# Performance work log

Measured on AMD Instinct MI355X. Metric: run time of the kernel, lower is better.

## Reference

```python
import jax, jax.numpy as jnp
import numpy as np

N_NODES = 100000
N_COMM = 1024
N_EDGES = 3200000
D_IN = 128
D_OUT = 128


def setup_inputs() -> dict:
    key = jax.random.key(0)
    k1, k2, k3, k4, k5, k6 = jax.random.split(key, 6)
    x = jax.random.normal(k1, (N_NODES + N_COMM, D_IN), dtype=jnp.float32)
    weight = jax.random.normal(k2, (D_IN, D_OUT), dtype=jnp.float32) * (1.0 / np.sqrt(D_IN))
    # assignments must be positive so row/col sums are nonzero
    assignments = jax.random.uniform(k3, (N_NODES, N_COMM), dtype=jnp.float32)
    edge_row = jax.random.randint(k4, (N_EDGES,), 0, N_NODES, dtype=jnp.int32)
    edge_col = jax.random.randint(k5, (N_EDGES,), 0, N_NODES, dtype=jnp.int32)
    edge_val = jax.random.uniform(k6, (N_EDGES,), dtype=jnp.float32)
    return {"x": x, "weight": weight, "assignments": assignments,
            "edge_row": edge_row, "edge_col": edge_col, "edge_val": edge_val}


def reference(x, weight, assignments, edge_row, edge_col, edge_val):
    N, C = assignments.shape
    support = x @ weight                      # [N+C, D_OUT]
    sup_nodes = support[:N]                   # node rows (support[:-C])
    sup_comm = support[N:]                    # community rows (support[-C:])

    # row-normalized assignments @ community support
    a_norm = assignments / assignments.sum(axis=1, keepdims=True)  # [N, C]
    comm_to_node = a_norm @ sup_comm                               # [N, D_OUT]

    # sparse adj @ node support via COO gather + segment scatter-add
    msgs = edge_val[:, None] * sup_nodes[edge_col]                 # [E, D_OUT]
    spmm = jax.ops.segment_sum(msgs, edge_row, num_segments=N)     # [N, D_OUT]

    output1 = comm_to_node + spmm                                  # [N, D_OUT]

    # row-normalized assignments.T @ node support
    at = assignments.T                                             # [C, N]
    at_norm = at / at.sum(axis=1, keepdims=True)
    output2 = at_norm @ sup_nodes                                  # [C, D_OUT]

    return jnp.concatenate((output1, output2), axis=0)            # [N+C, D_OUT]
```

## Files before the change

kernel.cpp:

```cpp
#include <hip/hip_runtime.h>

#define NN 100000
#define NC 1024
#define NM 101024
#define NE 3200000
#define DD 128

typedef __attribute__((ext_vector_type(8))) short s16x8;
typedef __attribute__((ext_vector_type(4))) float f32x4;

#define MFMA __builtin_amdgcn_mfma_f32_16x16x32_bf16

__device__ __forceinline__ short f2bf(float f) {
  unsigned u = __float_as_uint(f);
  u = (u + 0x7FFFu + ((u >> 16) & 1u)) >> 16;
  return (short)u;
}
__device__ __forceinline__ float bf2f(short h) {
  return __uint_as_float(((unsigned)(unsigned short)h) << 16);
}

__global__ __launch_bounds__(256) void k_zero(int* __restrict__ p, int n) {
  int t = blockIdx.x * 256 + threadIdx.x;
  if (t < n) p[t] = 0;
}

__global__ __launch_bounds__(256) void k_wpack(const float* __restrict__ W,
                                               short* __restrict__ wh,
                                               short* __restrict__ wl) {
  int t = blockIdx.x * 256 + threadIdx.x;
  int k = t >> 7, d = t & 127;
  float v = W[t];
  short h = f2bf(v);
  short l = f2bf(v - bf2f(h));
  int idx = (((k >> 5) * 8 + (d >> 4)) * 64 + ((k >> 3) & 3) * 16 + (d & 15)) * 8 + (k & 7);
  wh[idx] = h;
  wl[idx] = l;
}

__global__ __launch_bounds__(256) void k_support(const float* __restrict__ x,
                                                 const short* __restrict__ wh,
                                                 const short* __restrict__ wl,
                                                 float* __restrict__ sup) {
  int wave = threadIdx.x >> 6, lane = threadIdx.x & 63;
  int r0 = blockIdx.x * 64 + wave * 16;
  int arow = r0 + (lane & 15);
  if (arow >= NM) arow = NM - 1;
  int kb = (lane >> 4) * 8;
  f32x4 acc[8];
  #pragma unroll
  for (int dt = 0; dt < 8; ++dt)
    #pragma unroll
    for (int q = 0; q < 4; ++q) acc[dt][q] = 0.f;

  #pragma unroll
  for (int ks = 0; ks < 4; ++ks) {
    const float* ap = x + (size_t)arow * DD + ks * 32 + kb;
    float4 v0 = *(const float4*)ap;
    float4 v1 = *(const float4*)(ap + 4);
    float vv[8] = {v0.x, v0.y, v0.z, v0.w, v1.x, v1.y, v1.z, v1.w};
    s16x8 xh, xl;
    #pragma unroll
    for (int j = 0; j < 8; ++j) {
      short h = f2bf(vv[j]);
      xh[j] = h;
      xl[j] = f2bf(vv[j] - bf2f(h));
    }
    const short* bph = wh + ks * 4096 + lane * 8;
    const short* bpl = wl + ks * 4096 + lane * 8;
    #pragma unroll
    for (int dt = 0; dt < 8; ++dt) {
      s16x8 bh = *(const s16x8*)(bph + dt * 512);
      s16x8 bl = *(const s16x8*)(bpl + dt * 512);
      acc[dt] = MFMA(xh, bh, acc[dt], 0, 0, 0);
      acc[dt] = MFMA(xl, bh, acc[dt], 0, 0, 0);
      acc[dt] = MFMA(xh, bl, acc[dt], 0, 0, 0);
    }
  }
  int rg = (lane >> 4) * 4, cc = lane & 15;
  #pragma unroll
  for (int dt = 0; dt < 8; ++dt)
    #pragma unroll
    for (int q = 0; q < 4; ++q) {
      int rr = r0 + rg + q;
      if (rr < NM) sup[(size_t)rr * DD + dt * 16 + cc] = acc[dt][q];
    }
}

__global__ __launch_bounds__(256) void k_spack(const float* __restrict__ sup,
                                               short* __restrict__ bpk) {
  int t = blockIdx.x * 256 + threadIdx.x;
  int d = t & 127, ib = t >> 7;
  int rb = ib >> 2, g = ib & 3;
  s16x8 o;
  #pragma unroll
  for (int j = 0; j < 8; ++j) o[j] = f2bf(sup[(size_t)(ib * 8 + j) * DD + d]);
  *(s16x8*)(bpk + (size_t)((rb * 8 + (d >> 4)) * 64 + g * 16 + (d & 15)) * 8) = o;
}

__global__ __launch_bounds__(256) void k_u1(const float* __restrict__ A,
                                            const short* __restrict__ bpk,
                                            float* __restrict__ out) {
  __shared__ float rsh[128];
  int wave = threadIdx.x >> 6, lane = threadIdx.x & 63;
  int r0 = blockIdx.x * 128 + wave * 32;
  int kb = (lane >> 4) * 8;
  f32x4 acc[2][8];
  #pragma unroll
  for (int m = 0; m < 2; ++m)
    #pragma unroll
    for (int dt = 0; dt < 8; ++dt)
      #pragma unroll
      for (int q = 0; q < 4; ++q) acc[m][dt][q] = 0.f;
  float rs[2] = {0.f, 0.f};
  int row[2];
  #pragma unroll
  for (int m = 0; m < 2; ++m) {
    int r = r0 + m * 16 + (lane & 15);
    row[m] = (r < NN) ? r : NN - 1;
  }
  for (int ks = 0; ks < 32; ++ks) {
    s16x8 af[2];
    #pragma unroll
    for (int m = 0; m < 2; ++m) {
      const float* ap = A + (size_t)row[m] * NC + ks * 32 + kb;
      float4 v0 = *(const float4*)ap;
      float4 v1 = *(const float4*)(ap + 4);
      rs[m] += v0.x + v0.y + v0.z + v0.w + v1.x + v1.y + v1.z + v1.w;
      af[m][0] = f2bf(v0.x); af[m][1] = f2bf(v0.y);
      af[m][2] = f2bf(v0.z); af[m][3] = f2bf(v0.w);
      af[m][4] = f2bf(v1.x); af[m][5] = f2bf(v1.y);
      af[m][6] = f2bf(v1.z); af[m][7] = f2bf(v1.w);
    }
    const short* bp = bpk + (size_t)(3125 + ks) * 4096 + lane * 8;
    #pragma unroll
    for (int dt = 0; dt < 8; ++dt) {
      s16x8 b = *(const s16x8*)(bp + dt * 512);
      acc[0][dt] = MFMA(af[0], b, acc[0][dt], 0, 0, 0);
      acc[1][dt] = MFMA(af[1], b, acc[1][dt], 0, 0, 0);
    }
  }
  #pragma unroll
  for (int m = 0; m < 2; ++m) {
    float v = rs[m];
    v += __shfl_xor(v, 16);
    v += __shfl_xor(v, 32);
    if (lane < 16) rsh[wave * 32 + m * 16 + lane] = v;
  }
  __syncthreads();
  int rg = (lane >> 4) * 4, cc = lane & 15;
  #pragma unroll
  for (int m = 0; m < 2; ++m)
    #pragma unroll
    for (int q = 0; q < 4; ++q) {
      int wr = wave * 32 + m * 16 + rg + q;
      int r = blockIdx.x * 128 + wr;
      if (r < NN) {
        float inv = 1.f / rsh[wr];
        #pragma unroll
        for (int dt = 0; dt < 8; ++dt)
          out[(size_t)r * DD + dt * 16 + cc] = acc[m][dt][q] * inv;
      }
    }
}

__global__ __launch_bounds__(256) void k_u2(const float* __restrict__ A,
                                            const short* __restrict__ bpk,
                                            float* __restrict__ u2,
                                            float* __restrict__ csum) {
  __shared__ short atile[128 * 40];
  int wave = threadIdx.x >> 6, lane = threadIdx.x & 63;
  int c0 = (blockIdx.x & 7) * 128;
  int s = blockIdx.x >> 3;
  int wc = wave * 32;
  f32x4 acc[2][8];
  #pragma unroll
  for (int m = 0; m < 2; ++m)
    #pragma unroll
    for (int dt = 0; dt < 8; ++dt)
      #pragma unroll
      for (int q = 0; q < 4; ++q) acc[m][dt][q] = 0.f;
  float cs[2] = {0.f, 0.f};
  int ld_i = threadIdx.x >> 5;
  int ld_c = (threadIdx.x & 31) * 4;

  for (int kk = 0; kk < 25; ++kk) {
    int i0 = s * 800 + kk * 32;
    __syncthreads();
    #pragma unroll
    for (int it = 0; it < 4; ++it) {
      int i = it * 8 + ld_i;
      float4 v = *(const float4*)(A + (size_t)(i0 + i) * NC + c0 + ld_c);
      atile[(ld_c + 0) * 40 + i] = f2bf(v.x);
      atile[(ld_c + 1) * 40 + i] = f2bf(v.y);
      atile[(ld_c + 2) * 40 + i] = f2bf(v.z);
      atile[(ld_c + 3) * 40 + i] = f2bf(v.w);
    }
    __syncthreads();
    s16x8 af[2];
    #pragma unroll
    for (int m = 0; m < 2; ++m) {
      af[m] = *(const s16x8*)(atile + (wc + m * 16 + (lane & 15)) * 40 + (lane >> 4) * 8);
      #pragma unroll
      for (int j = 0; j < 8; ++j) cs[m] += bf2f(af[m][j]);
    }
    const short* bp = bpk + (size_t)(s * 25 + kk) * 4096 + lane * 8;
    #pragma unroll
    for (int dt = 0; dt < 8; ++dt) {
      s16x8 b = *(const s16x8*)(bp + dt * 512);
      acc[0][dt] = MFMA(af[0], b, acc[0][dt], 0, 0, 0);
      acc[1][dt] = MFMA(af[1], b, acc[1][dt], 0, 0, 0);
    }
  }
  #pragma unroll
  for (int m = 0; m < 2; ++m) {
    float v = cs[m];
    v += __shfl_xor(v, 16);
    v += __shfl_xor(v, 32);
    if (lane < 16) atomicAdd(&csum[c0 + wc + m * 16 + lane], v);
  }
  int rg = (lane >> 4) * 4, cc = lane & 15;
  #pragma unroll
  for (int m = 0; m < 2; ++m)
    #pragma unroll
    for (int dt = 0; dt < 8; ++dt)
      #pragma unroll
      for (int q = 0; q < 4; ++q)
        atomicAdd(&u2[(size_t)(c0 + wc + m * 16 + rg + q) * DD + dt * 16 + cc],
                  acc[m][dt][q]);
}

__global__ __launch_bounds__(256) void k_out2(const float* __restrict__ u2,
                                              const float* __restrict__ csum,
                                              float* __restrict__ out) {
  int t = blockIdx.x * 256 + threadIdx.x;
  int c = t >> 7;
  out[(size_t)(NN + c) * DD + (t & 127)] = u2[t] / csum[c];
}

__global__ __launch_bounds__(256) void k_hist(const int* __restrict__ er, int* __restrict__ hist) {
  int t = blockIdx.x * 256 + threadIdx.x;
  if (t < NE) atomicAdd(&hist[er[t]], 1);
}

__global__ __launch_bounds__(256) void k_scan1(const int* __restrict__ hist,
                                               int* __restrict__ excl,
                                               int* __restrict__ bsum) {
  __shared__ int sm[256];
  int t = threadIdx.x, g = blockIdx.x * 256 + t;
  int v = (g < NN) ? hist[g] : 0;
  sm[t] = v;
  __syncthreads();
  for (int off = 1; off < 256; off <<= 1) {
    int u = (t >= off) ? sm[t - off] : 0;
    __syncthreads();
    sm[t] += u;
    __syncthreads();
  }
  if (g < NN) excl[g] = sm[t] - v;
  if (t == 255) bsum[blockIdx.x] = sm[255];
}

__global__ __launch_bounds__(512) void k_scan2(const int* __restrict__ bsum,
                                               int* __restrict__ boff, int nb) {
  __shared__ int sm[512];
  int t = threadIdx.x;
  int v = (t < nb) ? bsum[t] : 0;
  sm[t] = v;
  __syncthreads();
  for (int off = 1; off < 512; off <<= 1) {
    int u = (t >= off) ? sm[t - off] : 0;
    __syncthreads();
    sm[t] += u;
    __syncthreads();
  }
  if (t < nb) boff[t] = sm[t] - v;
}

__global__ __launch_bounds__(256) void k_scan3(const int* __restrict__ excl,
                                               const int* __restrict__ boff,
                                               int* __restrict__ offs,
                                               int* __restrict__ cur) {
  int t = threadIdx.x, g = blockIdx.x * 256 + t;
  if (g < NN) {
    int o = excl[g] + boff[blockIdx.x];
    offs[g] = o;
    cur[g] = o;
  }
  if (g == 0) offs[NN] = NE;
}

__global__ __launch_bounds__(256) void k_scatter(const int* __restrict__ er,
                                                 const int* __restrict__ ec,
                                                 const float* __restrict__ ev,
                                                 int* __restrict__ cur,
                                                 int2* __restrict__ pairs) {
  int t = blockIdx.x * 256 + threadIdx.x;
  if (t < NE) {
    int r = er[t];
    int p = atomicAdd(&cur[r], 1);
    pairs[p] = make_int2(ec[t], __float_as_int(ev[t]));
  }
}

__global__ __launch_bounds__(256) void k_spmm(const int* __restrict__ offs,
                                              const int2* __restrict__ pairs,
                                              const float* __restrict__ sup,
                                              float* __restrict__ out) {
  int wave = threadIdx.x >> 6, lane = threadIdx.x & 63;
  int row = blockIdx.x * 4 + wave;
  int beg = offs[row], end = offs[row + 1];
  float ax = 0.f, ay = 0.f;
  for (int e = beg; e < end; ++e) {
    int2 p = pairs[e];
    float2 v = *(const float2*)(sup + (size_t)p.x * DD + lane * 2);
    float val = __int_as_float(p.y);
    ax = fmaf(val, v.x, ax);
    ay = fmaf(val, v.y, ay);
  }
  float2* o = (float2*)(out + (size_t)row * DD);
  float2 c = o[lane];
  c.x += ax;
  c.y += ay;
  o[lane] = c;
}

extern "C" void kernel_launch(void* const* d_in, const int* in_sizes, int n_in,
                              void* d_out, int out_size, void* d_ws, size_t ws_size,
                              hipStream_t stream) {
  const float* x  = (const float*)d_in[0];
  const float* W  = (const float*)d_in[1];
  const float* A  = (const float*)d_in[2];
  const int*   er = (const int*)d_in[3];
  const int*   ec = (const int*)d_in[4];
  const float* ev = (const float*)d_in[5];
  float* out = (float*)d_out;

  char* ws = (char*)d_ws;
  size_t off = 0;
  auto alloc = [&](size_t bytes) -> void* {
    off = (off + 255) & ~(size_t)255;
    void* p = ws + off;
    off += bytes;
    return p;
  };
  float* sup   = (float*)alloc((size_t)NM * DD * 4);
  short* bpk   = (short*)alloc((size_t)NM * DD * 2);
  short* wh    = (short*)alloc(128 * 128 * 2);
  short* wl    = (short*)alloc(128 * 128 * 2);
  float* u2    = (float*)alloc((size_t)NC * DD * 4);
  float* csum  = (float*)alloc(NC * 4);
  int*   hist  = (int*)alloc(NN * 4);
  int*   excl  = (int*)alloc(NN * 4);
  int*   offs  = (int*)alloc((NN + 1) * 4);
  int*   cur   = (int*)alloc(NN * 4);
  int*   bsum  = (int*)alloc(512 * 4);
  int*   boff  = (int*)alloc(512 * 4);
  int2*  pairs = (int2*)alloc((size_t)NE * 8);
  (void)ws_size; (void)in_sizes; (void)n_in; (void)out_size;

  const int ZN = NC * DD + NC + NN;
  k_zero<<<dim3((ZN + 255) / 256), dim3(256), 0, stream>>>((int*)u2, ZN);
  k_wpack<<<dim3(64), dim3(256), 0, stream>>>(W, wh, wl);
  k_support<<<dim3(1579), dim3(256), 0, stream>>>(x, wh, wl, sup);
  k_spack<<<dim3(6314), dim3(256), 0, stream>>>(sup, bpk);
  k_hist<<<dim3(12500), dim3(256), 0, stream>>>(er, hist);
  k_scan1<<<dim3(391), dim3(256), 0, stream>>>(hist, excl, bsum);
  k_scan2<<<dim3(1), dim3(512), 0, stream>>>(bsum, boff, 391);
  k_scan3<<<dim3(391), dim3(256), 0, stream>>>(excl, boff, offs, cur);
  k_scatter<<<dim3(12500), dim3(256), 0, stream>>>(er, ec, ev, cur, pairs);
  k_u1<<<dim3(782), dim3(256), 0, stream>>>(A, bpk, out);
  k_u2<<<dim3(1000), dim3(256), 0, stream>>>(A, bpk, u2, csum);
  k_out2<<<dim3(512), dim3(256), 0, stream>>>(u2, csum, out);
  k_spmm<<<dim3(25000), dim3(256), 0, stream>>>(offs, pairs, sup, out);
}
```

Before: 1.647 ms.

## Gather fp16 node support in SpMM, unroll edges, double-buffer k_u2 tiles

Adds a kernel that converts node support rows to packed fp16, and switches the SpMM gather to read these half-size rows, cutting random-gather bandwidth. The SpMM edge loop is unrolled by four so several gathers are in flight at once. k_u2 now double-buffers its LDS tile, prefetching the next A tile into registers while the current one is used, which removes one barrier per iteration. The costs are an extra conversion pass over the support matrix and fp16 rounding of the SpMM inputs, which adds precision loss.

```diff
diff --git a/kernel.cpp b/kernel.cpp
--- a/kernel.cpp
+++ b/kernel.cpp
@@ -1,4 +1,5 @@
 #include <hip/hip_runtime.h>
+#include <hip/hip_fp16.h>
 
 #define NN 100000
 #define NC 1024
@@ -87,6 +88,14 @@
     }
 }
 
+__global__ __launch_bounds__(256) void k_suph(const float* __restrict__ sup,
+                                              unsigned* __restrict__ suph) {
+  int t = blockIdx.x * 256 + threadIdx.x;
+  float2 f = *(const float2*)(sup + (size_t)t * 2);
+  __half2 h = __floats2half2_rn(f.x, f.y);
+  suph[t] = *(unsigned*)&h;
+}
+
 __global__ __launch_bounds__(256) void k_spack(const float* __restrict__ sup,
                                                short* __restrict__ bpk) {
   int t = blockIdx.x * 256 + threadIdx.x;
@@ -168,7 +177,7 @@
                                             const short* __restrict__ bpk,
                                             float* __restrict__ u2,
                                             float* __restrict__ csum) {
-  __shared__ short atile[128 * 40];
+  __shared__ short atile[2][128 * 40];
   int wave = threadIdx.x >> 6, lane = threadIdx.x & 63;
   int c0 = (blockIdx.x & 7) * 128;
   int s = blockIdx.x >> 3;
@@ -184,25 +193,44 @@
   int ld_i = threadIdx.x >> 5;
   int ld_c = (threadIdx.x & 31) * 4;
 
+  float4 rv[4];
+  #pragma unroll
+  for (int it = 0; it < 4; ++it)
+    rv[it] = *(const float4*)(A + (size_t)(s * 800 + it * 8 + ld_i) * NC + c0 + ld_c);
+  #pragma unroll
+  for (int it = 0; it < 4; ++it) {
+    int i = it * 8 + ld_i;
+    atile[0][(ld_c + 0) * 40 + i] = f2bf(rv[it].x);
+    atile[0][(ld_c + 1) * 40 + i] = f2bf(rv[it].y);
+    atile[0][(ld_c + 2) * 40 + i] = f2bf(rv[it].z);
+    atile[0][(ld_c + 3) * 40 + i] = f2bf(rv[it].w);
+  }
+  __syncthreads();
+
   for (int kk = 0; kk < 25; ++kk) {
-    int i0 = s * 800 + kk * 32;
-    __syncthreads();
-    #pragma unroll
-    for (int it = 0; it < 4; ++it) {
-      int i = it * 8 + ld_i;
-      float4 v = *(const float4*)(A + (size_t)(i0 + i) * NC + c0 + ld_c);
-      atile[(ld_c + 0) * 40 + i] = f2bf(v.x);
-      atile[(ld_c + 1) * 40 + i] = f2bf(v.y);
-      atile[(ld_c + 2) * 40 + i] = f2bf(v.z);
-      atile[(ld_c + 3) * 40 + i] = f2bf(v.w);
-    }
-    __syncthreads();
+    int p = kk & 1;
+    if (kk < 24) {
+      int i0n = s * 800 + (kk + 1) * 32;
+      #pragma unroll
+      for (int it = 0; it < 4; ++it)
+        rv[it] = *(const float4*)(A + (size_t)(i0n + it * 8 + ld_i) * NC + c0 + ld_c);
+    }
     s16x8 af[2];
     #pragma unroll
     for (int m = 0; m < 2; ++m) {
-      af[m] = *(const s16x8*)(atile + (wc + m * 16 + (lane & 15)) * 40 + (lane >> 4) * 8);
+      af[m] = *(const s16x8*)(&atile[p][(wc + m * 16 + (lane & 15)) * 40 + (lane >> 4) * 8]);
       #pragma unroll
       for (int j = 0; j < 8; ++j) cs[m] += bf2f(af[m][j]);
+    }
+    if (kk < 24) {
+      #pragma unroll
+      for (int it = 0; it < 4; ++it) {
+        int i = it * 8 + ld_i;
+        atile[p ^ 1][(ld_c + 0) * 40 + i] = f2bf(rv[it].x);
+        atile[p ^ 1][(ld_c + 1) * 40 + i] = f2bf(rv[it].y);
+        atile[p ^ 1][(ld_c + 2) * 40 + i] = f2bf(rv[it].z);
+        atile[p ^ 1][(ld_c + 3) * 40 + i] = f2bf(rv[it].w);
+      }
     }
     const short* bp = bpk + (size_t)(s * 25 + kk) * 4096 + lane * 8;
     #pragma unroll
@@ -211,6 +239,7 @@
       acc[0][dt] = MFMA(af[0], b, acc[0][dt], 0, 0, 0);
       acc[1][dt] = MFMA(af[1], b, acc[1][dt], 0, 0, 0);
     }
+    __syncthreads();
   }
   #pragma unroll
   for (int m = 0; m < 2; ++m) {
@@ -305,18 +334,37 @@
 
 __global__ __launch_bounds__(256) void k_spmm(const int* __restrict__ offs,
                                               const int2* __restrict__ pairs,
-                                              const float* __restrict__ sup,
+                                              const unsigned* __restrict__ suph,
                                               float* __restrict__ out) {
   int wave = threadIdx.x >> 6, lane = threadIdx.x & 63;
   int row = blockIdx.x * 4 + wave;
   int beg = offs[row], end = offs[row + 1];
   float ax = 0.f, ay = 0.f;
-  for (int e = beg; e < end; ++e) {
+  int e = beg;
+  for (; e + 4 <= end; e += 4) {
+    int2 p0 = pairs[e], p1 = pairs[e + 1], p2 = pairs[e + 2], p3 = pairs[e + 3];
+    unsigned g0 = suph[(size_t)p0.x * 64 + lane];
+    unsigned g1 = suph[(size_t)p1.x * 64 + lane];
+    unsigned g2 = suph[(size_t)p2.x * 64 + lane];
+    unsigned g3 = suph[(size_t)p3.x * 64 + lane];
+    float2 v0 = __half22float2(*(__half2*)&g0);
+    float2 v1 = __half22float2(*(__half2*)&g1);
+    float2 v2 = __half22float2(*(__half2*)&g2);
+    float2 v3 = __half22float2(*(__half2*)&g3);
+    float c0 = __int_as_float(p0.y), c1 = __int_as_float(p1.y);
+    float c2 = __int_as_float(p2.y), c3 = __int_as_float(p3.y);
+    ax = fmaf(c0, v0.x, ax); ay = fmaf(c0, v0.y, ay);
+    ax = fmaf(c1, v1.x, ax); ay = fmaf(c1, v1.y, ay);
+    ax = fmaf(c2, v2.x, ax); ay = fmaf(c2, v2.y, ay);
+    ax = fmaf(c3, v3.x, ax); ay = fmaf(c3, v3.y, ay);
+  }
+  for (; e < end; ++e) {
     int2 p = pairs[e];
-    float2 v = *(const float2*)(sup + (size_t)p.x * DD + lane * 2);
-    float val = __int_as_float(p.y);
-    ax = fmaf(val, v.x, ax);
-    ay = fmaf(val, v.y, ay);
+    unsigned g = suph[(size_t)p.x * 64 + lane];
+    float2 v = __half22float2(*(__half2*)&g);
+    float c = __int_as_float(p.y);
+    ax = fmaf(c, v.x, ax);
+    ay = fmaf(c, v.y, ay);
   }
   float2* o = (float2*)(out + (size_t)row * DD);
   float2 c = o[lane];
@@ -344,10 +392,11 @@
     off += bytes;
     return p;
   };
-  float* sup   = (float*)alloc((size_t)NM * DD * 4);
-  short* bpk   = (short*)alloc((size_t)NM * DD * 2);
-  short* wh    = (short*)alloc(128 * 128 * 2);
-  short* wl    = (short*)alloc(128 * 128 * 2);
+  float*    sup   = (float*)alloc((size_t)NM * DD * 4);
+  short*    bpk   = (short*)alloc((size_t)NM * DD * 2);
+  unsigned* suphp = (unsigned*)alloc((size_t)NN * 64 * 4);
+  short*    wh    = (short*)alloc(128 * 128 * 2);
+  short*    wl    = (short*)alloc(128 * 128 * 2);
   float* u2    = (float*)alloc((size_t)NC * DD * 4);
   float* csum  = (float*)alloc(NC * 4);
   int*   hist  = (int*)alloc(NN * 4);
@@ -363,6 +412,7 @@
   k_zero<<<dim3((ZN + 255) / 256), dim3(256), 0, stream>>>((int*)u2, ZN);
   k_wpack<<<dim3(64), dim3(256), 0, stream>>>(W, wh, wl);
   k_support<<<dim3(1579), dim3(256), 0, stream>>>(x, wh, wl, sup);
+  k_suph<<<dim3(25000), dim3(256), 0, stream>>>(sup, suphp);
   k_spack<<<dim3(6314), dim3(256), 0, stream>>>(sup, bpk);
   k_hist<<<dim3(12500), dim3(256), 0, stream>>>(er, hist);
   k_scan1<<<dim3(391), dim3(256), 0, stream>>>(hist, excl, bsum);
@@ -372,5 +422,5 @@
   k_u1<<<dim3(782), dim3(256), 0, stream>>>(A, bpk, out);
   k_u2<<<dim3(1000), dim3(256), 0, stream>>>(A, bpk, u2, csum);
   k_out2<<<dim3(512), dim3(256), 0, stream>>>(u2, csum, out);
-  k_spmm<<<dim3(25000), dim3(256), 0, stream>>>(offs, pairs, sup, out);
-}
+  k_spmm<<<dim3(25000), dim3(256), 0, stream>>>(offs, pairs, suphp, out);
+}
```

Measured after the change: 1.380 ms. -16.2%, faster.
